# Kernel tuning notes

Measured on AMD Instinct MI355X. Metric: run time of the kernel, lower is better.

## Reference

```python
import jax, jax.numpy as jnp
import numpy as np

DIM, ATT, G, T, KL, B = 1024, 128, 8, 4096, 256, 8
GD = DIM // G
SCALE = 1.0 / np.sqrt(ATT)

def setup_inputs() -> dict:
    key = jax.random.key(0)
    ks = jax.random.split(key, 7)
    x = jax.random.normal(ks[0], (B, T, DIM), dtype=jnp.float32)
    # stacked per-group weights (einsum orientation: in_dim x out_dim)
    Wq = jax.random.normal(ks[1], (G, GD, ATT), dtype=jnp.float32) * (1.0 / np.sqrt(GD))
    Wk = jax.random.normal(ks[2], (G, GD, ATT), dtype=jnp.float32) * (1.0 / np.sqrt(GD))
    Wv = jax.random.normal(ks[3], (G, GD, GD), dtype=jnp.float32) * (1.0 / np.sqrt(GD))
    Wo = jax.random.normal(ks[4], (G, GD, GD), dtype=jnp.float32) * (1.0 / np.sqrt(GD))
    Pk = jax.random.normal(ks[5], (G, T, KL), dtype=jnp.float32) * (1.0 / np.sqrt(T))
    Pv = jax.random.normal(ks[6], (G, T, KL), dtype=jnp.float32) * (1.0 / np.sqrt(T))
    return {"x": x, "Wq": Wq, "Wk": Wk, "Wv": Wv, "Wo": Wo, "Pk": Pk, "Pv": Pv}

def reference(x, Wq, Wk, Wv, Wo, Pk, Pv):
    Bx, Tx, _ = x.shape
    xg = x.reshape(Bx, Tx, G, GD).transpose(0, 2, 1, 3)        # [B,G,T,gd]
    q = jnp.einsum('bgtd,gda->bgta', xg, Wq)                   # [B,G,T,att]
    k = jnp.einsum('bgtd,gda->bgta', xg, Wk)
    v = jnp.einsum('bgtd,gde->bgte', xg, Wv)                   # [B,G,T,gd]
    k_red = jnp.einsum('bgta,gtk->bgka', k, Pk)                # [B,G,kl,att]
    v_red = jnp.einsum('bgte,gtk->bgke', v, Pv)                # [B,G,kl,gd]
    att = jax.nn.softmax(jnp.einsum('bgta,bgka->bgtk', q, k_red) * SCALE, axis=-1)
    out = jnp.einsum('bgtk,bgke->bgte', att, v_red)            # [B,G,T,gd]
    out = jnp.einsum('bgte,gef->bgtf', out, Wo)                # per-group output proj
    return out.transpose(0, 2, 1, 3).reshape(Bx, Tx, DIM)      # concat groups on last dim
```

## Files before the change

kernel.cpp:

```cpp
#include <hip/hip_runtime.h>
#include <hip/hip_bf16.h>

#define NB 8
#define NG 8
#define NT 4096
#define NDIM 1024
#define NGD 128
#define NATT 128
#define NKL 256
#define FSCALE 0.08838834764831845f

typedef __bf16 bf16x8 __attribute__((ext_vector_type(8)));
typedef float f32x4 __attribute__((ext_vector_type(4)));
typedef ushort u16x8 __attribute__((ext_vector_type(8)));
typedef ushort u16x4 __attribute__((ext_vector_type(4)));

#define MFMA(a, b, c) __builtin_amdgcn_mfma_f32_16x16x32_bf16(a, b, c, 0, 0, 0)

__device__ __forceinline__ ushort f2bf(float f) {
  union { float f; unsigned u; } v; v.f = f;
  unsigned r = v.u + 0x7FFFu + ((v.u >> 16) & 1u);
  return (ushort)(r >> 16);
}

__device__ __forceinline__ void gload16(const ushort* g, ushort* l) {
  __builtin_amdgcn_global_load_lds(
      (const __attribute__((address_space(1))) unsigned int*)g,
      (__attribute__((address_space(3))) unsigned int*)l, 16, 0, 0);
}

__global__ __launch_bounds__(512) void k0_weights(
    const float* __restrict__ Wq, const float* __restrict__ Wk,
    const float* __restrict__ Wv, const float* __restrict__ Wo,
    ushort* __restrict__ WkQT, ushort* __restrict__ WvoT) {
  const int sel = blockIdx.x;
  const int g = blockIdx.y;
  __shared__ float A2[128 * 136];
  __shared__ float B2[128 * 136];
  const int tid = threadIdx.x;

  if (sel == 0) {
#pragma unroll
    for (int u = 0; u < 8; ++u) {
      const int c = tid + 512 * u;
      const int row = c >> 5, c4 = (c & 31) * 4;
      *(float4*)&A2[row * 136 + c4] =
          *(const float4*)&Wo[(size_t)g * 16384 + row * 128 + c4];
      const float4 v = *(const float4*)&Wv[(size_t)g * 16384 + row * 128 + c4];
      B2[(c4 + 0) * 136 + row] = v.x;
      B2[(c4 + 1) * 136 + row] = v.y;
      B2[(c4 + 2) * 136 + row] = v.z;
      B2[(c4 + 3) * 136 + row] = v.w;
    }
  } else {
#pragma unroll
    for (int u = 0; u < 8; ++u) {
      const int c = tid + 512 * u;
      const int row = c >> 5, c4 = (c & 31) * 4;
      const float4 q = *(const float4*)&Wq[(size_t)g * 16384 + row * 128 + c4];
      A2[(c4 + 0) * 136 + row] = q.x;
      A2[(c4 + 1) * 136 + row] = q.y;
      A2[(c4 + 2) * 136 + row] = q.z;
      A2[(c4 + 3) * 136 + row] = q.w;
      const float4 k = *(const float4*)&Wk[(size_t)g * 16384 + row * 128 + c4];
      B2[(c4 + 0) * 136 + row] = k.x;
      B2[(c4 + 1) * 136 + row] = k.y;
      B2[(c4 + 2) * 136 + row] = k.z;
      B2[(c4 + 3) * 136 + row] = k.w;
    }
  }
  __syncthreads();

  const int mr = tid >> 4;
  const int mc = tid & 15;
  float acc[4][8];
#pragma unroll
  for (int i = 0; i < 4; ++i)
#pragma unroll
    for (int j = 0; j < 8; ++j) acc[i][j] = 0.f;

#pragma unroll 4
  for (int k = 0; k < 128; ++k) {
    const float4 a = *(const float4*)&A2[k * 136 + mr * 4];
    const float4 b0 = *(const float4*)&B2[k * 136 + mc * 8];
    const float4 b1 = *(const float4*)&B2[k * 136 + mc * 8 + 4];
    const float av[4] = {a.x, a.y, a.z, a.w};
    const float bv[8] = {b0.x, b0.y, b0.z, b0.w, b1.x, b1.y, b1.z, b1.w};
#pragma unroll
    for (int i = 0; i < 4; ++i)
#pragma unroll
      for (int j = 0; j < 8; ++j) acc[i][j] += av[i] * bv[j];
  }

  const float sc = sel ? FSCALE : 1.f;
  ushort* dst = (sel ? WkQT : WvoT) + (size_t)g * 16384;
#pragma unroll
  for (int i = 0; i < 4; ++i) {
    u16x8 pk;
#pragma unroll
    for (int j = 0; j < 8; ++j) pk[j] = f2bf(acc[i][j] * sc);
    *(u16x8*)&dst[(size_t)(mr * 4 + i) * 128 + mc * 8] = pk;
  }
}

__global__ __launch_bounds__(256) void kt_xp(
    const float* __restrict__ x, const float* __restrict__ Pk,
    const float* __restrict__ Pv, ushort* __restrict__ xT,
    ushort* __restrict__ PkT, ushort* __restrict__ PvT) {
  __shared__ float buf[64 * 132];
  const int bid = blockIdx.x;
  const int tid = threadIdx.x;

  if (bid < 4096) {
    const int t0 = (bid & 63) * 64;
    const int bg = bid >> 6;
    const int b = bg >> 3, g = bg & 7;
#pragma unroll
    for (int u = 0; u < 8; ++u) {
      const int c = tid + 256 * u;
      const int row = c >> 5, c4 = (c & 31) * 4;
      *(float4*)&buf[row * 132 + c4] =
          *(const float4*)&x[((size_t)b * NT + t0 + row) * NDIM + g * 128 + c4];
    }
    __syncthreads();
    const int seg = tid & 7;
    const int d0 = tid >> 3;
#pragma unroll
    for (int u = 0; u < 4; ++u) {
      const int d = d0 + u * 32;
      u16x8 pk;
#pragma unroll
      for (int z = 0; z < 8; ++z) pk[z] = f2bf(buf[(seg * 8 + z) * 132 + d]);
      *(u16x8*)&xT[((size_t)bg * 128 + d) * NT + t0 + seg * 8] = pk;
    }
  } else {
    const int idx = bid - 4096;
    const float* P = (idx >> 10) ? Pv : Pk;
    ushort* PT = (idx >> 10) ? PvT : PkT;
    const int r_ = idx & 1023;
    const int t0 = (r_ & 63) * 64;
    const int klh = (r_ >> 6) & 1;
    const int g = (r_ >> 7) & 7;
#pragma unroll
    for (int u = 0; u < 8; ++u) {
      const int c = tid + 256 * u;
      const int row = c >> 5, c4 = (c & 31) * 4;
      *(float4*)&buf[row * 132 + c4] =
          *(const float4*)&P[((size_t)g * NT + t0 + row) * NKL + klh * 128 + c4];
    }
    __syncthreads();
    const int seg = tid & 7;
    const int k0_ = tid >> 3;
#pragma unroll
    for (int u = 0; u < 4; ++u) {
      const int kl = k0_ + u * 32;
      u16x8 pk;
#pragma unroll
      for (int z = 0; z < 8; ++z) pk[z] = f2bf(buf[(seg * 8 + z) * 132 + kl]);
      *(u16x8*)&PT[((size_t)g * NKL + klh * 128 + kl) * NT + t0 + seg * 8] = pk;
    }
  }
}

__global__ __launch_bounds__(256, 2) void k1_mfma(
    const ushort* __restrict__ PkT, const ushort* __restrict__ PvT,
    const ushort* __restrict__ xT, const ushort* __restrict__ WkQT,
    const ushort* __restrict__ WvoT, ushort* __restrict__ MQ,
    ushort* __restrict__ vo_redT) {
  const int bid = blockIdx.x;
  const int work = (bid & 7) * 32 + (bid >> 3);
  const int bg = work >> 2;
  const int sel = (work >> 1) & 1;
  const int klt = work & 1;
  const int g = bg & 7;
  const ushort* PT = (sel ? PvT : PkT) + ((size_t)g * NKL + klt * 128) * NT;
  const ushort* Xb = xT + (size_t)bg * 128 * NT;

  __shared__ ushort lds[32768];

  const int tid = threadIdx.x;
  const int w = tid >> 6, lane = tid & 63;
  const int l15 = lane & 15, l4 = lane >> 4;
  const int rh = (w & 1) * 64;
  const int ch = (w >> 1) * 64;
  const int srow = lane >> 3, sc = lane & 7;

  f32x4 acc[4][4];
  const f32x4 fz = {0.f, 0.f, 0.f, 0.f};
#pragma unroll
  for (int i = 0; i < 4; ++i)
#pragma unroll
    for (int j = 0; j < 4; ++j) acc[i][j] = fz;

#define K1_STAGE(buf, s)                                                      \
  {                                                                           \
    const int t0_ = (s) * 64;                                                 \
    ushort* Ab_ = &lds[(buf) * 16384];                                        \
    ushort* Bb_ = &lds[(buf) * 16384 + 8192];                                 \
    _Pragma("unroll") for (int u = 0; u < 4; ++u) {                           \
      const int row_ = w * 32 + u * 8 + srow;                                 \
      const size_t off_ = (size_t)row_ * NT + t0_ + ((sc ^ (row_ & 7)) << 3); \
      gload16(PT + off_, Ab_ + (w * 32 + u * 8) * 64);                        \
      gload16(Xb + off_, Bb_ + (w * 32 + u * 8) * 64);                        \
    }                                                                         \
  }

#define K1_COMPUTE(buf)                                                       \
  {                                                                           \
    const ushort* Ab_ = &lds[(buf) * 16384];                                  \
    const ushort* Bb_ = &lds[(buf) * 16384 + 8192];                           \
    _Pragma("unroll") for (int h = 0; h < 2; ++h) {                           \
      bf16x8 af_[4], bf_[4];                                                  \
      _Pragma("unroll") for (int i = 0; i < 4; ++i) {                         \
        const int row_ = rh + i * 16 + l15;                                   \
        af_[i] = *(const bf16x8*)&Ab_[row_ * 64 +                             \
                                      (((h * 4 + l4) ^ (row_ & 7)) << 3)];    \
      }                                                                       \
      _Pragma("unroll") for (int j = 0; j < 4; ++j) {                         \
        const int row_ = ch + j * 16 + l15;                                   \
        bf_[j] = *(const bf16x8*)&Bb_[row_ * 64 +                             \
                                      (((h * 4 + l4) ^ (row_ & 7)) << 3)];    \
      }                                                                       \
      _Pragma("unroll") for (int i = 0; i < 4; ++i)                           \
        _Pragma("unroll") for (int j = 0; j < 4; ++j)                         \
          acc[i][j] = MFMA(af_[i], bf_[j], acc[i][j]);                        \
    }                                                                         \
  }

  K1_STAGE(0, 0);
  __syncthreads();
  int buf = 0;
#pragma unroll 1
  for (int s = 0; s < 64; ++s) {
    if (s + 1 < 64) K1_STAGE(buf ^ 1, s + 1);
    K1_COMPUTE(buf);
    __syncthreads();
    buf ^= 1;
  }

  ushort* C = lds;
#pragma unroll
  for (int i = 0; i < 4; ++i)
#pragma unroll
    for (int j = 0; j < 4; ++j)
#pragma unroll
      for (int r = 0; r < 4; ++r)
        C[(rh + i * 16 + l4 * 4 + r) * 136 + ch + j * 16 + l15] =
            f2bf(acc[i][j][r]);
  __syncthreads();

  const ushort* WT = (sel ? WvoT : WkQT) + (size_t)g * 16384;
  f32x4 o[4][4];
#pragma unroll
  for (int i = 0; i < 4; ++i)
#pragma unroll
    for (int j = 0; j < 4; ++j) o[i][j] = fz;
#pragma unroll
  for (int ks = 0; ks < 4; ++ks) {
    bf16x8 af[4], bfr[4];
#pragma unroll
    for (int i = 0; i < 4; ++i)
      af[i] = *(const bf16x8*)&C[(rh + i * 16 + l15) * 136 + ks * 32 + l4 * 8];
#pragma unroll
    for (int j = 0; j < 4; ++j)
      bfr[j] = *(const bf16x8*)&WT[(size_t)(ch + j * 16 + l15) * 128 + ks * 32 + l4 * 8];
#pragma unroll
    for (int i = 0; i < 4; ++i)
#pragma unroll
      for (int j = 0; j < 4; ++j) o[i][j] = MFMA(af[i], bfr[j], o[i][j]);
  }

  if (sel == 0) {
#pragma unroll
    for (int i = 0; i < 4; ++i)
#pragma unroll
      for (int j = 0; j < 4; ++j)
#pragma unroll
        for (int r = 0; r < 4; ++r)
          MQ[((size_t)bg * NKL + klt * 128 + rh + i * 16 + l4 * 4 + r) * 128 +
             ch + j * 16 + l15] = f2bf(o[i][j][r]);
  } else {
#pragma unroll
    for (int i = 0; i < 4; ++i)
#pragma unroll
      for (int j = 0; j < 4; ++j) {
        u16x4 pk;
#pragma unroll
        for (int r = 0; r < 4; ++r) pk[r] = f2bf(o[i][j][r]);
        *(u16x4*)&vo_redT[((size_t)bg * 128 + ch + j * 16 + l15) * NKL +
                          klt * 128 + rh + i * 16 + l4 * 4] = pk;
      }
  }
}

__global__ __launch_bounds__(512, 2) void k2_attn(
    const float* __restrict__ x, const ushort* __restrict__ MQ,
    const ushort* __restrict__ vo_redT, float* __restrict__ out) {
  const int id = blockIdx.x;
  const int bg = id & 63;
  const int tc = id >> 6;
  const int b = bg >> 3, g = bg & 7;

  __shared__ ushort mq[256 * 136];
  __shared__ ushort att[64 * 264];
  __shared__ float redm[2][64];
  __shared__ float reds[2][64];

  const int tid = threadIdx.x;
  const int w = tid >> 6, lane = tid & 63;
  const int l15 = lane & 15, l4 = lane >> 4;
  const int tw = w >> 1, half = w & 1;
  const f32x4 fz = {0.f, 0.f, 0.f, 0.f};

  {
    const ushort* src = MQ + (size_t)bg * NKL * 128;
#pragma unroll
    for (int u = 0; u < 8; ++u) {
      const int c = tid + 512 * u;
      const int r = c >> 4, c8 = (c & 15) * 8;
      *(u16x8*)&mq[r * 136 + c8] = *(const u16x8*)&src[r * 128 + c8];
    }
  }

  const float* xb = x + ((size_t)b * NT + tc * 512) * NDIM + g * 128;
  const ushort* vo = vo_redT + ((size_t)bg * 128 + half * 64) * NKL;

  float4 xr[8];
#pragma unroll
  for (int ks = 0; ks < 4; ++ks) {
    const float* p = xb + (size_t)(tw * 16 + l15) * NDIM + ks * 32 + l4 * 8;
    xr[ks * 2] = *(const float4*)p;
    xr[ks * 2 + 1] = *(const float4*)(p + 4);
  }
  __syncthreads();

#pragma unroll 1
  for (int st = 0; st < 8; ++st) {
    bf16x8 a[4];
#pragma unroll
    for (int ks = 0; ks < 4; ++ks) {
      bf16x8 t;
      t[0] = (__bf16)xr[ks * 2].x; t[1] = (__bf16)xr[ks * 2].y;
      t[2] = (__bf16)xr[ks * 2].z; t[3] = (__bf16)xr[ks * 2].w;
      t[4] = (__bf16)xr[ks * 2 + 1].x; t[5] = (__bf16)xr[ks * 2 + 1].y;
      t[6] = (__bf16)xr[ks * 2 + 1].z; t[7] = (__bf16)xr[ks * 2 + 1].w;
      a[ks] = t;
    }
    if (st + 1 < 8) {
      const float* pn = xb + (size_t)((st + 1) * 64 + tw * 16 + l15) * NDIM;
#pragma unroll
      for (int ks = 0; ks < 4; ++ks) {
        xr[ks * 2] = *(const float4*)(pn + ks * 32 + l4 * 8);
        xr[ks * 2 + 1] = *(const float4*)(pn + ks * 32 + l4 * 8 + 4);
      }
    }
    f32x4 s[8];
#pragma unroll
    for (int n = 0; n < 8; ++n) s[n] = fz;
#pragma unroll
    for (int n = 0; n < 8; ++n) {
      const int row = (half * 8 + n) * 16 + l15;
#pragma unroll
      for (int ks = 0; ks < 4; ++ks) {
        const bf16x8 bv = *(const bf16x8*)&mq[row * 136 + ks * 32 + l4 * 8];
        s[n] = MFMA(a[ks], bv, s[n]);
      }
    }
    const int rowbase = tw * 16 + l4 * 4;
    float inv[4];
    {
      float mx[4];
#pragma unroll
      for (int r = 0; r < 4; ++r) {
        float m = s[0][r];
#pragma unroll
        for (int n = 1; n < 8; ++n) m = fmaxf(m, s[n][r]);
#pragma unroll
        for (int off = 1; off < 16; off <<= 1) m = fmaxf(m, __shfl_xor(m, off, 64));
        mx[r] = m;
      }
      if (l15 == 0) {
#pragma unroll
        for (int r = 0; r < 4; ++r) redm[half][rowbase + r] = mx[r];
      }
      __syncthreads();
      float sm[4];
#pragma unroll
      for (int r = 0; r < 4; ++r) {
        const float mg = fmaxf(mx[r], redm[half ^ 1][rowbase + r]);
        float acc = 0.f;
#pragma unroll
        for (int n = 0; n < 8; ++n) {
          const float p = __expf(s[n][r] - mg);
          acc += p;
          att[(rowbase + r) * 264 + (half * 8 + n) * 16 + l15] = f2bf(p);
        }
#pragma unroll
        for (int off = 1; off < 16; off <<= 1) acc += __shfl_xor(acc, off, 64);
        sm[r] = acc;
      }
      if (l15 == 0) {
#pragma unroll
        for (int r = 0; r < 4; ++r) reds[half][rowbase + r] = sm[r];
      }
      __syncthreads();
#pragma unroll
      for (int r = 0; r < 4; ++r)
        inv[r] = 1.f / (sm[r] + reds[half ^ 1][rowbase + r]);
    }
    f32x4 oa[4];
#pragma unroll
    for (int j = 0; j < 4; ++j) oa[j] = fz;
#pragma unroll
    for (int ks = 0; ks < 8; ++ks) {
      const bf16x8 av = *(const bf16x8*)&att[(tw * 16 + l15) * 264 + ks * 32 + l4 * 8];
#pragma unroll
      for (int j = 0; j < 4; ++j) {
        const bf16x8 bv = *(const bf16x8*)&vo[(size_t)(j * 16 + l15) * NKL + ks * 32 + l4 * 8];
        oa[j] = MFMA(av, bv, oa[j]);
      }
    }
    float* ob = out + ((size_t)b * NT + tc * 512 + st * 64 + tw * 16) * NDIM +
                g * 128 + half * 64;
#pragma unroll
    for (int j = 0; j < 4; ++j)
#pragma unroll
      for (int r = 0; r < 4; ++r)
        ob[(size_t)(l4 * 4 + r) * NDIM + j * 16 + l15] = oa[j][r] * inv[r];
  }
}

extern "C" void kernel_launch(void* const* d_in, const int* in_sizes, int n_in,
                              void* d_out, int out_size, void* d_ws, size_t ws_size,
                              hipStream_t stream) {
  (void)in_sizes; (void)n_in; (void)out_size; (void)ws_size;
  const float* x  = (const float*)d_in[0];
  const float* Wq = (const float*)d_in[1];
  const float* Wk = (const float*)d_in[2];
  const float* Wv = (const float*)d_in[3];
  const float* Wo = (const float*)d_in[4];
  const float* Pk = (const float*)d_in[5];
  const float* Pv = (const float*)d_in[6];

  ushort* wsu = (ushort*)d_ws;
  ushort* PkT     = wsu;
  ushort* PvT     = PkT + 8388608;
  ushort* WkQT    = PvT + 8388608;
  ushort* WvoT    = WkQT + 131072;
  ushort* MQ      = WvoT + 131072;
  ushort* vo_redT = MQ + 2097152;
  ushort* xT = (ushort*)d_out;

  k0_weights<<<dim3(2, NG), dim3(512), 0, stream>>>(Wq, Wk, Wv, Wo, WkQT, WvoT);
  kt_xp<<<dim3(4096 + 2048), dim3(256), 0, stream>>>(x, Pk, Pv, xT, PkT, PvT);
  k1_mfma<<<dim3(256), dim3(256), 0, stream>>>(PkT, PvT, xT, WkQT, WvoT,
                                               MQ, vo_redT);
  k2_attn<<<dim3(512), dim3(512), 0, stream>>>(x, MQ, vo_redT, (float*)d_out);
}
```

Before: 233.4 us.

## Use per-half local softmax max and double-buffered att to drop one barrier

Each half-block now computes exp with its own local row max instead of waiting for the global max, so the max and sum exchange share a single barrier per step. The attention probability buffer and the reduction arrays are double-buffered by step parity, which removes the hazard between the next step's writes and the current step's reads. The PV product is split into two accumulators, one per key half, and these are rescaled by their respective max-correction factors at output time. The cost is more LDS use, which may limit occupancy at two blocks per CU, and slightly different rounding because bf16 probabilities are now computed against a local max.

```diff
diff --git a/kernel.cpp b/kernel.cpp
--- a/kernel.cpp
+++ b/kernel.cpp
@@ -302,9 +302,9 @@
   const int b = bg >> 3, g = bg & 7;
 
   __shared__ ushort mq[256 * 136];
-  __shared__ ushort att[64 * 264];
-  __shared__ float redm[2][64];
-  __shared__ float reds[2][64];
+  __shared__ ushort att[2][64 * 264];
+  __shared__ float redm[2][2][64];
+  __shared__ float reds[2][2][64];
 
   const int tid = threadIdx.x;
   const int w = tid >> 6, lane = tid & 63;
@@ -336,6 +336,8 @@
 
 #pragma unroll 1
   for (int st = 0; st < 8; ++st) {
+    const int pb = st & 1;
+    ushort* attb = att[pb];
     bf16x8 a[4];
 #pragma unroll
     for (int ks = 0; ks < 4; ++ks) {
@@ -367,57 +369,66 @@
       }
     }
     const int rowbase = tw * 16 + l4 * 4;
-    float inv[4];
-    {
-      float mx[4];
+    float mx[4], sm[4];
+#pragma unroll
+    for (int r = 0; r < 4; ++r) {
+      float m = s[0][r];
+#pragma unroll
+      for (int n = 1; n < 8; ++n) m = fmaxf(m, s[n][r]);
+#pragma unroll
+      for (int off = 1; off < 16; off <<= 1) m = fmaxf(m, __shfl_xor(m, off, 64));
+      mx[r] = m;
+    }
+#pragma unroll
+    for (int r = 0; r < 4; ++r) {
+      float acc = 0.f;
+#pragma unroll
+      for (int n = 0; n < 8; ++n) {
+        const float p = __expf(s[n][r] - mx[r]);
+        acc += p;
+        attb[(rowbase + r) * 264 + (half * 8 + n) * 16 + l15] = f2bf(p);
+      }
+#pragma unroll
+      for (int off = 1; off < 16; off <<= 1) acc += __shfl_xor(acc, off, 64);
+      sm[r] = acc;
+    }
+    if (l15 == 0) {
 #pragma unroll
       for (int r = 0; r < 4; ++r) {
-        float m = s[0][r];
-#pragma unroll
-        for (int n = 1; n < 8; ++n) m = fmaxf(m, s[n][r]);
-#pragma unroll
-        for (int off = 1; off < 16; off <<= 1) m = fmaxf(m, __shfl_xor(m, off, 64));
-        mx[r] = m;
-      }
-      if (l15 == 0) {
-#pragma unroll
-        for (int r = 0; r < 4; ++r) redm[half][rowbase + r] = mx[r];
-      }
-      __syncthreads();
-      float sm[4];
-#pragma unroll
-      for (int r = 0; r < 4; ++r) {
-        const float mg = fmaxf(mx[r], redm[half ^ 1][rowbase + r]);
-        float acc = 0.f;
-#pragma unroll
-        for (int n = 0; n < 8; ++n) {
-          const float p = __expf(s[n][r] - mg);
-          acc += p;
-          att[(rowbase + r) * 264 + (half * 8 + n) * 16 + l15] = f2bf(p);
-        }
-#pragma unroll
-        for (int off = 1; off < 16; off <<= 1) acc += __shfl_xor(acc, off, 64);
-        sm[r] = acc;
-      }
-      if (l15 == 0) {
-#pragma unroll
-        for (int r = 0; r < 4; ++r) reds[half][rowbase + r] = sm[r];
-      }
-      __syncthreads();
-#pragma unroll
-      for (int r = 0; r < 4; ++r)
-        inv[r] = 1.f / (sm[r] + reds[half ^ 1][rowbase + r]);
-    }
-    f32x4 oa[4];
-#pragma unroll
-    for (int j = 0; j < 4; ++j) oa[j] = fz;
-#pragma unroll
-    for (int ks = 0; ks < 8; ++ks) {
-      const bf16x8 av = *(const bf16x8*)&att[(tw * 16 + l15) * 264 + ks * 32 + l4 * 8];
+        redm[pb][half][rowbase + r] = mx[r];
+        reds[pb][half][rowbase + r] = sm[r];
+      }
+    }
+    __syncthreads();
+    float sc_me[4], sc_ot[4], inv[4];
+#pragma unroll
+    for (int r = 0; r < 4; ++r) {
+      const float mo = redm[pb][half ^ 1][rowbase + r];
+      const float lo = reds[pb][half ^ 1][rowbase + r];
+      const float mg = fmaxf(mx[r], mo);
+      sc_me[r] = __expf(mx[r] - mg);
+      sc_ot[r] = __expf(mo - mg);
+      inv[r] = 1.f / (sm[r] * sc_me[r] + lo * sc_ot[r]);
+    }
+    f32x4 oa0[4], oa1[4];
+#pragma unroll
+    for (int j = 0; j < 4; ++j) { oa0[j] = fz; oa1[j] = fz; }
+#pragma unroll
+    for (int ks = 0; ks < 4; ++ks) {
+      const bf16x8 av = *(const bf16x8*)&attb[(tw * 16 + l15) * 264 + ks * 32 + l4 * 8];
 #pragma unroll
       for (int j = 0; j < 4; ++j) {
         const bf16x8 bv = *(const bf16x8*)&vo[(size_t)(j * 16 + l15) * NKL + ks * 32 + l4 * 8];
-        oa[j] = MFMA(av, bv, oa[j]);
+        oa0[j] = MFMA(av, bv, oa0[j]);
+      }
+    }
+#pragma unroll
+    for (int ks = 4; ks < 8; ++ks) {
+      const bf16x8 av = *(const bf16x8*)&attb[(tw * 16 + l15) * 264 + ks * 32 + l4 * 8];
+#pragma unroll
+      for (int j = 0; j < 4; ++j) {
+        const bf16x8 bv = *(const bf16x8*)&vo[(size_t)(j * 16 + l15) * NKL + ks * 32 + l4 * 8];
+        oa1[j] = MFMA(av, bv, oa1[j]);
       }
     }
     float* ob = out + ((size_t)b * NT + tc * 512 + st * 64 + tw * 16) * NDIM +
@@ -425,8 +436,12 @@
 #pragma unroll
     for (int j = 0; j < 4; ++j)
 #pragma unroll
-      for (int r = 0; r < 4; ++r)
-        ob[(size_t)(l4 * 4 + r) * NDIM + j * 16 + l15] = oa[j][r] * inv[r];
+      for (int r = 0; r < 4; ++r) {
+        const float f0 = half ? sc_ot[r] : sc_me[r];
+        const float f1 = half ? sc_me[r] : sc_ot[r];
+        ob[(size_t)(l4 * 4 + r) * NDIM + j * 16 + l15] =
+            (oa0[j][r] * f0 + oa1[j][r] * f1) * inv[r];
+      }
   }
 }
 
```

Result: slower. 241.8 us (+3.6%).
